# Performance work log

Hardware: AMD Instinct MI355X
Metric: run time of the kernel (lower is better)

Reference implementation:

```python
import jax, jax.numpy as jnp
import numpy as np

B, S, H, E, V, T = 64, 256, 1024, 512, 10000, 64
D = H // 2  # per-direction LSTM hidden


def setup_inputs() -> dict:
    key = jax.random.key(0)
    ks = jax.random.split(key, 16)
    s = jnp.float32(0.02)
    emb = jax.random.normal(ks[4], (V, E), jnp.float32) * s
    emb = emb.at[0].set(0.0)  # padding_idx=0
    return {
        "encoder_outputs": jax.random.normal(ks[0], (B, S, H), jnp.float32),
        "enc_h0": jax.random.normal(ks[1], (2, B, D), jnp.float32),
        "enc_c0": jax.random.normal(ks[2], (2, B, D), jnp.float32),
        "target": jax.random.randint(ks[3], (B, T), 1, V),
        "mask": jnp.zeros((B, S), jnp.bool_),
        "sos_idx": 1,
        "emb": emb,
        "Wa": jax.random.normal(ks[5], (H, H), jnp.float32) * s,
        "Ua": jax.random.normal(ks[6], (H, H), jnp.float32) * s,
        "Va": jax.random.normal(ks[7], (H,), jnp.float32) * s,
        "out_W": jax.random.normal(ks[8], (V, H), jnp.float32) * s,
        "out_b": jnp.zeros((V,), jnp.float32),
        "Wih_f": jax.random.normal(ks[9], (4 * D, E + H), jnp.float32) * s,
        "Whh_f": jax.random.normal(ks[10], (4 * D, D), jnp.float32) * s,
        "bih_f": jnp.zeros((4 * D,), jnp.float32),
        "bhh_f": jnp.zeros((4 * D,), jnp.float32),
        "Wih_b": jax.random.normal(ks[11], (4 * D, E + H), jnp.float32) * s,
        "Whh_b": jax.random.normal(ks[12], (4 * D, D), jnp.float32) * s,
        "bih_b": jnp.zeros((4 * D,), jnp.float32),
        "bhh_b": jnp.zeros((4 * D,), jnp.float32),
    }


def _lstm_cell(x, h, c, Wih, Whh, bih, bhh):
    g = x @ Wih.T + h @ Whh.T + bih + bhh
    i, f, gg, o = jnp.split(g, 4, axis=-1)  # torch gate order i,f,g,o
    c2 = jax.nn.sigmoid(f) * c + jax.nn.sigmoid(i) * jnp.tanh(gg)
    h2 = jax.nn.sigmoid(o) * jnp.tanh(c2)
    return h2, c2


def reference(encoder_outputs, enc_h0, enc_c0, target, mask, sos_idx, emb, Wa, Ua, Va,
              out_W, out_b, Wih_f, Whh_f, bih_f, bhh_f, Wih_b, Whh_b, bih_b, bhh_b):
    # Cache Ua(keys) once (original recomputes it each step; math identical).
    Uk = jnp.einsum('bsh,kh->bsk', encoder_outputs, Ua)  # [B,S,H]
    b = encoder_outputs.shape[0]
    tokens = jnp.concatenate(
        [jnp.full((b, 1), sos_idx, target.dtype), target[:, :-1]], axis=1)  # [B,T]
    xs = tokens.T  # [T,B]

    def step(carry, tok):
        h, c = carry  # each [2,B,D]
        query = jnp.swapaxes(h, 0, 1).reshape(b, -1)  # [B,H] (fwd||bwd)
        sc = jnp.einsum('bsh,h->bs', jnp.tanh((query @ Wa.T)[:, None, :] + Uk), Va)
        sc = jnp.where(mask, -jnp.inf, sc)
        w = jax.nn.softmax(sc, axis=-1)  # [B,S]
        ctx = jnp.einsum('bs,bsh->bh', w, encoder_outputs)  # [B,H]
        x = jnp.concatenate([emb[tok], ctx], axis=-1)  # [B,E+H]
        hf, cf = _lstm_cell(x, h[0], c[0], Wih_f, Whh_f, bih_f, bhh_f)
        hb, cb = _lstm_cell(x, h[1], c[1], Wih_b, Whh_b, bih_b, bhh_b)
        out = jnp.concatenate([hf, hb], axis=-1)  # [B,H]
        logits = out @ out_W.T + out_b  # [B,V]
        return (jnp.stack([hf, hb]), jnp.stack([cf, cb])), (logits, w)

    (h, c), (logits, attns) = jax.lax.scan(step, (enc_h0, enc_c0), xs)
    decoder_outputs = jnp.swapaxes(logits, 0, 1)  # [B,T,V]
    attentions = jnp.swapaxes(attns, 0, 1)        # [B,T,S]
    return decoder_outputs, h, c, attentions
```

## Files before the change

kernel.cpp:

```cpp
#include <hip/hip_runtime.h>

#define NB 64
#define NS 256
#define NH 1024
#define NE 512
#define NV 10000
#define NT 64
#define ND 512
#define NEH 1536
#define HST (65 * NH)

typedef __attribute__((ext_vector_type(8))) short bf16x8;
typedef __attribute__((ext_vector_type(4))) float f32x4;

__device__ __forceinline__ short F2B(float f) {
  unsigned u = __float_as_uint(f);
  return (short)((u + 0x7fffu + ((u >> 16) & 1u)) >> 16);
}
__device__ __forceinline__ float B2F(short s) {
  return __uint_as_float(((unsigned)(unsigned short)s) << 16);
}
__device__ __forceinline__ float ftanh(float x) {
  float e = __expf(2.f * x);
  return 1.f - 2.f * __builtin_amdgcn_rcpf(e + 1.f);
}

#define GLD16(src, dst)                                                        \
  __builtin_amdgcn_global_load_lds(                                            \
      (const __attribute__((address_space(1))) void*)(src),                    \
      (__attribute__((address_space(3))) void*)(dst), 16, 0, 0)

__device__ __forceinline__ void mm64_f32a(
    const float* __restrict__ Af, int lda, const short* __restrict__ Wg,
    int ldw, int K, short* Ch, size_t ldc, char* smem)
{
  const int tid = threadIdx.x;
  const int lane = tid & 63, w = tid >> 6;
  const int qm = (w >> 1) << 5, qn = (w & 1) << 5;
  const int kg = lane >> 4, rl = lane & 15;
  f32x4 acc[2][2] = {};
  const int nIt = K >> 6;

  auto stage = [&](int k0, int buf) {
    char* As = smem + (buf << 14);
    char* Bs = As + 8192;
#pragma unroll
    for (int p = 0; p < 2; ++p) {
      int j = tid + (p << 8);
      int row = j >> 3;
      int c = (j & 7) ^ (row & 7);
      const float* src = Af + (size_t)row * lda + k0 + (c << 3);
      float4 v0 = ((const float4*)src)[0];
      float4 v1 = ((const float4*)src)[1];
      bf16x8 pk;
      pk[0] = F2B(v0.x); pk[1] = F2B(v0.y); pk[2] = F2B(v0.z); pk[3] = F2B(v0.w);
      pk[4] = F2B(v1.x); pk[5] = F2B(v1.y); pk[6] = F2B(v1.z); pk[7] = F2B(v1.w);
      *((bf16x8*)As + j) = pk;
    }
#pragma unroll
    for (int p = 0; p < 2; ++p) {
      int j = (w << 7) + (p << 6) + lane;
      int row = j >> 3;
      int c = (j & 7) ^ (row & 7);
      GLD16(Wg + (size_t)row * ldw + k0 + (c << 3), Bs + (w << 11) + (p << 10));
    }
  };

  stage(0, 0);
  for (int it = 0; it < nIt; ++it) {
    __syncthreads();
    if (it + 1 < nIt) stage((it + 1) << 6, (it + 1) & 1);
    const short* As = (const short*)(smem + ((it & 1) << 14));
    const short* Bs = As + 4096;
#pragma unroll
    for (int kk = 0; kk < 2; ++kk) {
      bf16x8 af[2], bfr[2];
#pragma unroll
      for (int mt = 0; mt < 2; ++mt) {
        int r2 = qm + (mt << 4) + rl;
        int c = (kk << 2) + kg;
        af[mt] = *((const bf16x8*)As + ((r2 << 3) | (c ^ (r2 & 7))));
      }
#pragma unroll
      for (int nt = 0; nt < 2; ++nt) {
        int r2 = qn + (nt << 4) + rl;
        int c = (kk << 2) + kg;
        bfr[nt] = *((const bf16x8*)Bs + ((r2 << 3) | (c ^ (r2 & 7))));
      }
#pragma unroll
      for (int mt = 0; mt < 2; ++mt)
#pragma unroll
        for (int nt = 0; nt < 2; ++nt)
          acc[mt][nt] = __builtin_amdgcn_mfma_f32_16x16x32_bf16(
              af[mt], bfr[nt], acc[mt][nt], 0, 0, 0);
    }
  }
#pragma unroll
  for (int mt = 0; mt < 2; ++mt)
#pragma unroll
    for (int nt = 0; nt < 2; ++nt) {
      int cn = qn + (nt << 4) + rl;
#pragma unroll
      for (int r = 0; r < 4; ++r) {
        int rowm = qm + (mt << 4) + (kg << 2) + r;
        Ch[(size_t)rowm * ldc + cn] = F2B(acc[mt][nt][r]);
      }
    }
}

__global__ __launch_bounds__(256) void uk_mm_f32(const float* __restrict__ enc,
                                                 const short* __restrict__ Ua_h,
                                                 short* __restrict__ Uk_h) {
  __shared__ char smem[32768];
  mm64_f32a(enc + (size_t)blockIdx.y * 64 * NH, NH,
            Ua_h + (size_t)blockIdx.x * 64 * NH, NH, NH,
            Uk_h + (size_t)blockIdx.y * 64 * NH + blockIdx.x * 64, NH, smem);
}

template <int MODE>
__global__ __launch_bounds__(256) void mm128p(
    const short* __restrict__ A, const short* __restrict__ Bw, int nvmax,
    const float* __restrict__ bias, float* __restrict__ Cf,
    short* __restrict__ Ch)
{
  __shared__ char smem[65536];
  const int tid = threadIdx.x, lane = tid & 63, w = tid >> 6;
  const int m0 = blockIdx.y << 7;
  const int n0 = blockIdx.x << 7;
  const int qm = (w >> 1) << 6, qn = (w & 1) << 6;
  const int kg = lane >> 4, rl = lane & 15;
  f32x4 acc[4][4] = {};

  auto stage = [&](int it, int buf) {
    char* dst = smem + (buf << 15);
    const int k0 = it << 6;
#pragma unroll
    for (int p = 0; p < 4; ++p) {
      int j = (((w << 2) + p) << 6) + lane;
      int row = j >> 3;
      int c = (j & 7) ^ (row & 7);
      int m = m0 + row;
      size_t arow = (MODE == 0) ? ((size_t)(m >> 6) * 65 + (m & 63) + 1)
                                : (size_t)m;
      GLD16(A + arow * NH + k0 + (c << 3), dst + (((w << 2) + p) << 10));
      int vr = n0 + row; if (vr > nvmax - 1) vr = nvmax - 1;
      GLD16(Bw + (size_t)vr * NH + k0 + (c << 3),
            dst + 16384 + (((w << 2) + p) << 10));
    }
  };

  stage(0, 0); stage(1, 1);
  for (int it = 0; it < 16; ++it) {
    if (it < 15) asm volatile("s_waitcnt vmcnt(8)" ::: "memory");
    else         asm volatile("s_waitcnt vmcnt(0)" ::: "memory");
    __builtin_amdgcn_s_barrier();
    __builtin_amdgcn_sched_barrier(0);
    const short* As = (const short*)(smem + ((it & 1) << 15));
    const short* Bs = As + 8192;
#pragma unroll
    for (int kk = 0; kk < 2; ++kk) {
      bf16x8 af[4], bfr[4];
#pragma unroll
      for (int mt = 0; mt < 4; ++mt) {
        int r2 = qm + (mt << 4) + rl;
        int c = (kk << 2) + kg;
        af[mt] = *((const bf16x8*)As + ((r2 << 3) | (c ^ (r2 & 7))));
      }
#pragma unroll
      for (int nt = 0; nt < 4; ++nt) {
        int r2 = qn + (nt << 4) + rl;
        int c = (kk << 2) + kg;
        bfr[nt] = *((const bf16x8*)Bs + ((r2 << 3) | (c ^ (r2 & 7))));
      }
#pragma unroll
      for (int mt = 0; mt < 4; ++mt)
#pragma unroll
        for (int nt = 0; nt < 4; ++nt)
          acc[mt][nt] = __builtin_amdgcn_mfma_f32_16x16x32_bf16(
              af[mt], bfr[nt], acc[mt][nt], 0, 0, 0);
    }
    __builtin_amdgcn_sched_barrier(0);
    __builtin_amdgcn_s_barrier();
    if (it + 2 < 16) stage(it + 2, it & 1);
  }
#pragma unroll
  for (int nt = 0; nt < 4; ++nt) {
    int colv = n0 + qn + (nt << 4) + rl;
    if (colv < nvmax) {
#pragma unroll
      for (int mt = 0; mt < 4; ++mt)
#pragma unroll
        for (int r = 0; r < 4; ++r) {
          int m = m0 + qm + (mt << 4) + (kg << 2) + r;
          if (MODE == 0) {
            Cf[(size_t)m * NV + colv] = acc[mt][nt][r] + bias[colv];
          } else {
            Ch[(size_t)m * NH + colv] = F2B(acc[mt][nt][r]);
          }
        }
    }
  }
}

__global__ __launch_bounds__(256) void gates_v2(
    const short* __restrict__ Xt, const short* __restrict__ hcur,
    const short* __restrict__ Wcomb, const float* __restrict__ bperm,
    const float* __restrict__ cq_old, float* __restrict__ hq_f,
    float* __restrict__ cq_new, short* __restrict__ hnext)
{
  __shared__ char smem[61440];
  const int tid = threadIdx.x, lane = tid & 63, w = tid >> 6;
  const int kg = lane >> 4, rl = lane & 15;
  const int dir = blockIdx.x >> 7, gi = blockIdx.x & 127;
  const int hoff = dir << 9;
  const short* Wbase = Wcomb + (((size_t)(dir << 11) + (gi << 4)) << 11);

  auto stage = [&](int it, int buf) {
    char* dst = smem + buf * 20480;
#pragma unroll
    for (int g = 0; g < 4; ++g) {
      int row = (g << 4) + (w << 2) + kg;
      int c = rl ^ (row & 15);
      int k = (it << 7) + (c << 3);
      const short* src = (k < NEH)
          ? (Xt + (size_t)row * NEH + k)
          : (hcur + (size_t)row * HST + hoff + (k - NEH));
      GLD16(src, dst + (g << 12) + (w << 10));
    }
    {
      int rowB = (w << 2) + kg;
      int cB = rl ^ rowB;
      int kB = (it << 7) + (cB << 3);
      GLD16(Wbase + (size_t)rowB * 2048 + kB, dst + 16384 + (w << 10));
    }
  };

  stage(0, 0); stage(1, 1); stage(2, 2);
  f32x4 acc = {};
  int buf = 0;
  for (int it = 0; it < 16; ++it) {
    if (it < 14)      asm volatile("s_waitcnt vmcnt(10)" ::: "memory");
    else if (it == 14) asm volatile("s_waitcnt vmcnt(5)" ::: "memory");
    else               asm volatile("s_waitcnt vmcnt(0)" ::: "memory");
    __builtin_amdgcn_s_barrier();
    __builtin_amdgcn_sched_barrier(0);
    const short* As = (const short*)(smem + buf * 20480);
    const short* Bs = (const short*)(smem + buf * 20480 + 16384);
    const int rowA = (w << 4) + rl;
#pragma unroll
    for (int kk = 0; kk < 4; ++kk) {
      int chunk = (kk << 2) | kg;
      bf16x8 af = *((const bf16x8*)As + ((rowA << 4) | (chunk ^ (rowA & 15))));
      bf16x8 bf = *((const bf16x8*)Bs + ((rl << 4) | (chunk ^ rl)));
      acc = __builtin_amdgcn_mfma_f32_16x16x32_bf16(af, bf, acc, 0, 0, 0);
    }
    __builtin_amdgcn_sched_barrier(0);
    __builtin_amdgcn_s_barrier();
    if (it + 3 < 16) stage(it + 3, buf);
    buf = (buf == 2) ? 0 : buf + 1;
  }
  float* gacc = (float*)smem;
#pragma unroll
  for (int r = 0; r < 4; ++r)
    gacc[((w << 4) + (kg << 2) + r) * 17 + rl] = acc[r];
  __syncthreads();
  {
    const int b = tid >> 2, j2 = tid & 3;
    const float* bp = bperm + (dir << 11) + (gi << 4) + (j2 << 2);
    const float* gr = gacc + b * 17 + (j2 << 2);
    float gi_ = gr[0] + bp[0];
    float gf_ = gr[1] + bp[1];
    float gg_ = gr[2] + bp[2];
    float go_ = gr[3] + bp[3];
    const int d = ((gi >> 2) << 4) + (((gi << 2) + j2) & 15);
    const int idx = (b << 10) + hoff + d;
    float c0v = cq_old[idx];
    float si = 1.f / (1.f + __expf(-gi_));
    float sf = 1.f / (1.f + __expf(-gf_));
    float so = 1.f / (1.f + __expf(-go_));
    float tg = ftanh(gg_);
    float c2 = sf * c0v + si * tg;
    float h2 = so * ftanh(c2);
    hq_f[idx] = h2;
    cq_new[idx] = c2;
    hnext[(size_t)b * HST + hoff + d] = F2B(h2);
  }
}

__global__ __launch_bounds__(256) void q_mm2(const short* __restrict__ hcur,
                                             const short* __restrict__ Wa_h,
                                             float* __restrict__ q)
{
  __shared__ char smem[61440];
  const int tid = threadIdx.x, lane = tid & 63, w = tid >> 6;
  const int kg = lane >> 4, rl = lane & 15;
  const int n0 = blockIdx.x << 4;
  const short* Wbase = Wa_h + (size_t)n0 * NH;

  auto stage = [&](int it, int buf) {
    char* dst = smem + buf * 20480;
#pragma unroll
    for (int g = 0; g < 4; ++g) {
      int row = (g << 4) + (w << 2) + kg;
      int c = rl ^ (row & 15);
      int k = (it << 7) + (c << 3);
      GLD16(hcur + (size_t)row * HST + k, dst + (g << 12) + (w << 10));
    }
    {
      int rowB = (w << 2) + kg;
      int cB = rl ^ rowB;
      int kB = (it << 7) + (cB << 3);
      GLD16(Wbase + (size_t)rowB * NH + kB, dst + 16384 + (w << 10));
    }
  };

  stage(0, 0); stage(1, 1); stage(2, 2);
  f32x4 acc = {};
  int buf = 0;
  for (int it = 0; it < 8; ++it) {
    if (it < 6)       asm volatile("s_waitcnt vmcnt(10)" ::: "memory");
    else if (it == 6) asm volatile("s_waitcnt vmcnt(5)" ::: "memory");
    else              asm volatile("s_waitcnt vmcnt(0)" ::: "memory");
    __builtin_amdgcn_s_barrier();
    __builtin_amdgcn_sched_barrier(0);
    const short* As = (const short*)(smem + buf * 20480);
    const short* Bs = (const short*)(smem + buf * 20480 + 16384);
    const int rowA = (w << 4) + rl;
#pragma unroll
    for (int kk = 0; kk < 4; ++kk) {
      int chunk = (kk << 2) | kg;
      bf16x8 af = *((const bf16x8*)As + ((rowA << 4) | (chunk ^ (rowA & 15))));
      bf16x8 bf = *((const bf16x8*)Bs + ((rl << 4) | (chunk ^ rl)));
      acc = __builtin_amdgcn_mfma_f32_16x16x32_bf16(af, bf, acc, 0, 0, 0);
    }
    __builtin_amdgcn_sched_barrier(0);
    __builtin_amdgcn_s_barrier();
    if (it + 3 < 8) stage(it + 3, buf);
    buf = (buf == 2) ? 0 : buf + 1;
  }
#pragma unroll
  for (int r = 0; r < 4; ++r)
    q[(size_t)((w << 4) + (kg << 2) + r) * NH + n0 + rl] = acc[r];
}

__global__ __launch_bounds__(256) void f2b_k(const float* __restrict__ in,
                                             short* __restrict__ out, int n4) {
  int i = blockIdx.x * 256 + threadIdx.x;
  const int stride = gridDim.x * 256;
  for (; i < n4; i += stride) {
    float4 v = ((const float4*)in)[i];
    short4 o;
    o.x = F2B(v.x); o.y = F2B(v.y); o.z = F2B(v.z); o.w = F2B(v.w);
    ((short4*)out)[i] = o;
  }
}

__global__ __launch_bounds__(256) void f2b2_k(
    const float* __restrict__ in0, short* __restrict__ out0,
    const float* __restrict__ in1, short* __restrict__ out1, int n4each) {
  int i = blockIdx.x * 256 + threadIdx.x;
  const int stride = gridDim.x * 256;
  for (; i < 2 * n4each; i += stride) {
    const float* in = (i < n4each) ? in0 : in1;
    short* out = (i < n4each) ? out0 : out1;
    int j = (i < n4each) ? i : i - n4each;
    float4 v = ((const float4*)in)[j];
    short4 o;
    o.x = F2B(v.x); o.y = F2B(v.y); o.z = F2B(v.z); o.w = F2B(v.w);
    ((short4*)out)[j] = o;
  }
}

__global__ __launch_bounds__(256) void perm_w(
    const float* __restrict__ Wih_f, const float* __restrict__ Whh_f,
    const float* __restrict__ Wih_b, const float* __restrict__ Whh_b,
    const float* __restrict__ bih_f, const float* __restrict__ bhh_f,
    const float* __restrict__ bih_b, const float* __restrict__ bhh_b,
    short* __restrict__ Wcomb, float* __restrict__ bias_perm)
{
  int i = blockIdx.x * 256 + threadIdx.x;
  int k4 = i & 511;
  int np = (i >> 9) & 2047;
  int dir = i >> 20;
  int gate = np & 3, dlo = (np >> 2) & 15, dblk = np >> 6;
  int d = (dblk << 4) + dlo;
  int r = (gate << 9) + d;
  int k = k4 << 2;
  const float* Wih = dir ? Wih_b : Wih_f;
  const float* Whh = dir ? Whh_b : Whh_f;
  float4 v = (k < NEH) ? *(const float4*)(Wih + (size_t)r * NEH + k)
                       : *(const float4*)(Whh + (size_t)r * ND + (k - NEH));
  short4 o;
  o.x = F2B(v.x); o.y = F2B(v.y); o.z = F2B(v.z); o.w = F2B(v.w);
  *(short4*)(Wcomb + ((size_t)((dir << 11) + np) << 11) + k) = o;
  if (k4 == 0) {
    const float* bi = dir ? bih_b : bih_f;
    const float* bh = dir ? bhh_b : bhh_f;
    bias_perm[(dir << 11) + np] = bi[r] + bh[r];
  }
}

__global__ __launch_bounds__(256) void emb_fill(
    const float* __restrict__ emb, const int* __restrict__ target,
    const int* __restrict__ sos, short* __restrict__ Xbuf)
{
  int idx = blockIdx.x * 256 + threadIdx.x;
  int t = idx >> 13;
  int r = idx & 8191;
  int b = r >> 7, e4 = r & 127;
  int tok = (t == 0) ? sos[0] : target[b * NT + t - 1];
  float4 v = *(const float4*)(emb + (size_t)tok * NE + (e4 << 2));
  short4 o;
  o.x = F2B(v.x); o.y = F2B(v.y); o.z = F2B(v.z); o.w = F2B(v.w);
  *(short4*)(Xbuf + (size_t)(t * NB + b) * NEH + (e4 << 2)) = o;
}

__global__ __launch_bounds__(256) void init_state(
    const float* __restrict__ h0, const float* __restrict__ c0,
    float* __restrict__ hq, float* __restrict__ cq, short* __restrict__ H0) {
  int idx = blockIdx.x * 256 + threadIdx.x;
  int b = idx >> 10, dir = (idx >> 9) & 1, d = idx & 511;
  int src = dir * NB * ND + (b << 9) + d;
  float h = h0[src];
  hq[idx] = h;
  cq[idx] = c0[src];
  H0[(size_t)b * HST + (dir << 9) + d] = F2B(h);
}

__global__ __launch_bounds__(256) void final_state(
    const float* __restrict__ hq, const float* __restrict__ cq,
    float* __restrict__ out_h, float* __restrict__ out_c) {
  int idx = blockIdx.x * 256 + threadIdx.x;
  int dir = idx >> 15, r = idx & 32767, b = r >> 9, d = r & 511;
  int src = b * NH + dir * ND + d;
  out_h[idx] = hq[src];
  out_c[idx] = cq[src];
}

__global__ __launch_bounds__(256) void attn_score(
    const float* __restrict__ q, const short* __restrict__ Uk,
    const float* __restrict__ Va, const unsigned char* __restrict__ mask,
    float* __restrict__ sc) {
  __shared__ float qs[NH];
  const int b = blockIdx.x >> 6;
  {
    int t4 = threadIdx.x << 2;
    *(float4*)(qs + t4) = *(const float4*)(q + (size_t)b * NH + t4);
  }
  __syncthreads();
  const int lane = threadIdx.x & 63, wid = threadIdx.x >> 6;
  const int bs = (blockIdx.x << 2) + wid;
  const short* ukp = Uk + (size_t)bs * NH;
  float acc = 0.f;
#pragma unroll
  for (int i = 0; i < 2; ++i) {
    int h = (i << 9) + (lane << 3);
    bf16x8 uv = *(const bf16x8*)(ukp + h);
    float4 q0 = *(const float4*)(qs + h);
    float4 q1 = *(const float4*)(qs + h + 4);
    float4 v0 = *(const float4*)(Va + h);
    float4 v1 = *(const float4*)(Va + h + 4);
    acc += v0.x * ftanh(q0.x + B2F(uv[0]));
    acc += v0.y * ftanh(q0.y + B2F(uv[1]));
    acc += v0.z * ftanh(q0.z + B2F(uv[2]));
    acc += v0.w * ftanh(q0.w + B2F(uv[3]));
    acc += v1.x * ftanh(q1.x + B2F(uv[4]));
    acc += v1.y * ftanh(q1.y + B2F(uv[5]));
    acc += v1.z * ftanh(q1.z + B2F(uv[6]));
    acc += v1.w * ftanh(q1.w + B2F(uv[7]));
  }
#pragma unroll
  for (int o = 32; o; o >>= 1) acc += __shfl_down(acc, o);
  if (lane == 0) sc[bs] = mask[bs] ? -__builtin_inff() : acc;
}

__global__ __launch_bounds__(512) void ctx_soft(
    const float* __restrict__ sc, const short* __restrict__ enc_h,
    const float* __restrict__ enc_f, int use_h,
    short* __restrict__ Xt, float* __restrict__ attn_out, int t) {
  const int tid = threadIdx.x;
  const int b = blockIdx.x >> 2, qh = blockIdx.x & 3;
  __shared__ float red[8];
  __shared__ float ws[NS];
  __shared__ float4 red4[512];
  const int s8 = tid & 255;
  float v = sc[b * NS + s8];
  float m = v;
#pragma unroll
  for (int o = 32; o; o >>= 1) m = fmaxf(m, __shfl_down(m, o));
  if ((tid & 63) == 0) red[tid >> 6] = m;
  __syncthreads();
  m = fmaxf(fmaxf(fmaxf(red[0], red[1]), fmaxf(red[2], red[3])),
            fmaxf(fmaxf(red[4], red[5]), fmaxf(red[6], red[7])));
  float e = __expf(v - m);
  float su = e;
#pragma unroll
  for (int o = 32; o; o >>= 1) su += __shfl_down(su, o);
  __syncthreads();
  if ((tid & 63) == 0) red[tid >> 6] = su;
  __syncthreads();
  su = red[0] + red[1] + red[2] + red[3];
  float wgt = e / su;
  ws[s8] = wgt;
  if (qh == 0 && tid < 256) attn_out[((size_t)b * NT + t) * NS + tid] = wgt;
  __syncthreads();
  const int w8 = tid >> 6, l = tid & 63;
  const int h = (qh << 8) + (l << 2);
  const int s0 = w8 << 5;
  float4 a = make_float4(0.f, 0.f, 0.f, 0.f);
  if (use_h) {
    const short* ep = enc_h + ((size_t)b * NS + s0) * NH + h;
    for (int s = 0; s < 32; ++s) {
      short4 vv = *(const short4*)(ep + (size_t)s * NH);
      float wv = ws[s0 + s];
      a.x += wv * B2F(vv.x); a.y += wv * B2F(vv.y);
      a.z += wv * B2F(vv.z); a.w += wv * B2F(vv.w);
    }
  } else {
    const float* ep = enc_f + ((size_t)b * NS + s0) * NH + h;
    for (int s = 0; s < 32; ++s) {
      float4 vv = *(const float4*)(ep + (size_t)s * NH);
      float wv = ws[s0 + s];
      a.x += wv * vv.x; a.y += wv * vv.y; a.z += wv * vv.z; a.w += wv * vv.w;
    }
  }
  red4[(w8 << 6) + l] = a;
  __syncthreads();
  if (tid < 64) {
    float sx = 0.f, sy = 0.f, sz = 0.f, sw = 0.f;
#pragma unroll
    for (int k = 0; k < 8; ++k) {
      float4 r = red4[(k << 6) + tid];
      sx += r.x; sy += r.y; sz += r.z; sw += r.w;
    }
    short4 o;
    o.x = F2B(sx); o.y = F2B(sy); o.z = F2B(sz); o.w = F2B(sw);
    *(short4*)(Xt + (size_t)b * NEH + NE + (qh << 8) + (tid << 2)) = o;
  }
}

extern "C" void kernel_launch(void* const* d_in, const int* in_sizes, int n_in,
                              void* d_out, int out_size, void* d_ws, size_t ws_size,
                              hipStream_t stream)
{
  const float* enc    = (const float*)d_in[0];
  const float* h0     = (const float*)d_in[1];
  const float* c0     = (const float*)d_in[2];
  const int*   target = (const int*)d_in[3];
  const unsigned char* mask = (const unsigned char*)d_in[4];
  const int*   sos    = (const int*)d_in[5];
  const float* emb    = (const float*)d_in[6];
  const float* Wa     = (const float*)d_in[7];
  const float* Ua     = (const float*)d_in[8];
  const float* Va     = (const float*)d_in[9];
  const float* out_W  = (const float*)d_in[10];
  const float* out_b  = (const float*)d_in[11];
  const float* Wih_f  = (const float*)d_in[12];
  const float* Whh_f  = (const float*)d_in[13];
  const float* bih_f  = (const float*)d_in[14];
  const float* bhh_f  = (const float*)d_in[15];
  const float* Wih_b  = (const float*)d_in[16];
  const float* Whh_b  = (const float*)d_in[17];
  const float* bih_b  = (const float*)d_in[18];
  const float* bhh_b  = (const float*)d_in[19];

  float* out_dec  = (float*)d_out;
  float* out_h    = out_dec + (size_t)NB * NT * NV;
  float* out_c    = out_h + 2 * NB * ND;
  float* out_attn = out_c + 2 * NB * ND;

  char* base = (char*)d_ws;
  size_t off = 0;
  auto alloc = [&](size_t bytes) -> char* {
    char* p = base + off;
    off += (bytes + 255) & ~(size_t)255;
    return p;
  };
  short* Uk_h  = (short*)alloc((size_t)NB * NS * NH * 2);
  short* ow_h  = (short*)alloc((size_t)NV * NH * 2);
  short* Ua_h  = (short*)alloc((size_t)NH * NH * 2);
  short* Wa_h  = (short*)alloc((size_t)NH * NH * 2);
  short* Wcomb = (short*)alloc((size_t)2 * 2048 * 2048 * 2);
  float* bperm = (float*)alloc((size_t)2 * 2048 * 4);
  float* q     = (float*)alloc((size_t)NB * NH * 4);
  float* sc    = (float*)alloc((size_t)NB * NS * 4);
  short* Xbuf  = (short*)alloc((size_t)NT * NB * NEH * 2);
  float* hq    = (float*)alloc((size_t)NB * NH * 4);
  float* cq    = (float*)alloc((size_t)2 * NB * NH * 4);
  short* Hbuf  = (short*)alloc((size_t)NB * HST * 2);
  short* enc_h = nullptr;
  int use_h = 0;
  if (off + (size_t)NB * NS * NH * 2 <= ws_size) {
    enc_h = (short*)alloc((size_t)NB * NS * NH * 2);
    use_h = 1;
  }
  if (off > ws_size) return;

  f2b_k<<<dim3(2048), dim3(256), 0, stream>>>(out_W, ow_h, NV * NH / 4);
  f2b2_k<<<dim3(2048), dim3(256), 0, stream>>>(Ua, Ua_h, Wa, Wa_h, NH * NH / 4);
  perm_w<<<dim3(8192), dim3(256), 0, stream>>>(Wih_f, Whh_f, Wih_b, Whh_b,
                                               bih_f, bhh_f, bih_b, bhh_b,
                                               Wcomb, bperm);
  emb_fill<<<dim3(2048), dim3(256), 0, stream>>>(emb, target, sos, Xbuf);
  init_state<<<dim3(256), dim3(256), 0, stream>>>(h0, c0, hq, cq, Hbuf);
  if (use_h) {
    f2b_k<<<dim3(2048), dim3(256), 0, stream>>>(enc, enc_h, NB * NS * NH / 4);
    mm128p<1><<<dim3(8, 128), dim3(256), 0, stream>>>(enc_h, Ua_h, NH, nullptr,
                                                      nullptr, Uk_h);
  } else {
    uk_mm_f32<<<dim3(16, 256), dim3(256), 0, stream>>>(enc, Ua_h, Uk_h);
  }

  for (int t = 0; t < NT; ++t) {
    const short* hcur = Hbuf + (size_t)t * NH;
    short* hnext = Hbuf + (size_t)(t + 1) * NH;
    float* cq_cur = cq + (t & 1) * (NB * NH);
    float* cq_nxt = cq + ((t & 1) ^ 1) * (NB * NH);
    short* Xt = Xbuf + (size_t)t * NB * NEH;

    q_mm2<<<dim3(64), dim3(256), 0, stream>>>(hcur, Wa_h, q);
    attn_score<<<dim3(4096), dim3(256), 0, stream>>>(q, Uk_h, Va, mask, sc);
    ctx_soft<<<dim3(256), dim3(512), 0, stream>>>(sc, enc_h, enc, use_h,
                                                  Xt, out_attn, t);
    gates_v2<<<dim3(256), dim3(256), 0, stream>>>(Xt, hcur, Wcomb, bperm,
                                                  cq_cur, hq, cq_nxt, hnext);
  }

  mm128p<0><<<dim3(79, 32), dim3(256), 0, stream>>>(Hbuf, ow_h, NV,
                                                    out_b, out_dec, nullptr);
  final_state<<<dim3(256), dim3(256), 0, stream>>>(hq, cq, out_h, out_c);
}
```

Before: 2.127 ms.

## Fuse attention score, softmax and context into one kernel with inter-block barrier

```diff
diff --git a/kernel.cpp b/kernel.cpp
--- a/kernel.cpp
+++ b/kernel.cpp
@@ -125,8 +125,8 @@
 {
   __shared__ char smem[65536];
   const int tid = threadIdx.x, lane = tid & 63, w = tid >> 6;
-  const int m0 = blockIdx.y << 7;
-  const int n0 = blockIdx.x << 7;
+  const int m0 = blockIdx.x << 7;
+  const int n0 = blockIdx.y << 7;
   const int qm = (w >> 1) << 6, qn = (w & 1) << 6;
   const int kg = lane >> 4, rl = lane & 15;
   f32x4 acc[4][4] = {};
@@ -199,6 +199,122 @@
           }
         }
     }
+  }
+}
+
+__global__ __launch_bounds__(512) void attn_one(
+    const float* __restrict__ q, const short* __restrict__ Uk,
+    const float* __restrict__ Va, const unsigned char* __restrict__ mask,
+    const short* __restrict__ enc_h, const float* __restrict__ enc_f,
+    int use_h, short* __restrict__ Xt, float* __restrict__ attn_out,
+    unsigned* __restrict__ ebuf, unsigned* __restrict__ cnt, int t)
+{
+  __shared__ float qs[NH];
+  __shared__ float vas[NH];
+  __shared__ float eall[NS];
+  __shared__ float wsm[NS];
+  __shared__ float4 red4[512];
+  __shared__ float redsum;
+  const int tid = threadIdx.x;
+  const int b = blockIdx.x >> 2, part = blockIdx.x & 3;
+  const int lane = tid & 63, w = tid >> 6;
+
+  {
+    int i2 = tid << 1;
+    *(float2*)(qs + i2) = *(const float2*)(q + (size_t)b * NH + i2);
+    *(float2*)(vas + i2) = *(const float2*)(Va + i2);
+  }
+  __syncthreads();
+
+#pragma unroll 1
+  for (int i = 0; i < 8; ++i) {
+    const int s = (part << 6) + (w << 3) + i;
+    const short* up = Uk + ((size_t)b * NS + s) * NH + (lane << 4);
+    bf16x8 u0 = ((const bf16x8*)up)[0];
+    bf16x8 u1 = ((const bf16x8*)up)[1];
+    const float* qp = qs + (lane << 4);
+    const float* vp = vas + (lane << 4);
+    float a = 0.f;
+#pragma unroll
+    for (int j = 0; j < 8; ++j) a += vp[j] * ftanh(qp[j] + B2F(u0[j]));
+#pragma unroll
+    for (int j = 0; j < 8; ++j) a += vp[8 + j] * ftanh(qp[8 + j] + B2F(u1[j]));
+#pragma unroll
+    for (int o = 32; o; o >>= 1) a += __shfl_down(a, o);
+    if (lane == 0) {
+      float e = mask[b * NS + s] ? 0.f : __expf(a);
+      __hip_atomic_store(&ebuf[b * NS + s], __float_as_uint(e),
+                         __ATOMIC_RELAXED, __HIP_MEMORY_SCOPE_AGENT);
+    }
+  }
+  asm volatile("s_waitcnt vmcnt(0)" ::: "memory");
+  __syncthreads();
+  if (tid == 0) {
+    __hip_atomic_fetch_add(&cnt[b << 4], 1u, __ATOMIC_RELAXED,
+                           __HIP_MEMORY_SCOPE_AGENT);
+    const unsigned tgt = 4u * (unsigned)(t + 1);
+    while (__hip_atomic_load(&cnt[b << 4], __ATOMIC_RELAXED,
+                             __HIP_MEMORY_SCOPE_AGENT) < tgt)
+      __builtin_amdgcn_s_sleep(8);
+  }
+  __syncthreads();
+  if (tid < NS)
+    eall[tid] = __uint_as_float(__hip_atomic_load(
+        &ebuf[b * NS + tid], __ATOMIC_RELAXED, __HIP_MEMORY_SCOPE_AGENT));
+  __syncthreads();
+  if (w == 0) {
+    float su = eall[lane] + eall[lane + 64] + eall[lane + 128] +
+               eall[lane + 192];
+#pragma unroll
+    for (int o = 32; o; o >>= 1) su += __shfl_down(su, o);
+    if (lane == 0) redsum = su;
+  }
+  __syncthreads();
+  {
+    float inv = 1.f / redsum;
+    if (tid < NS) {
+      float ww = eall[tid] * inv;
+      wsm[tid] = ww;
+      if (part == 0) attn_out[((size_t)b * NT + t) * NS + tid] = ww;
+    }
+  }
+  __syncthreads();
+
+  const int w8 = tid >> 6, l = tid & 63;
+  const int h = (part << 8) + (l << 2);
+  const int s0 = w8 << 5;
+  float4 a4 = make_float4(0.f, 0.f, 0.f, 0.f);
+  if (use_h) {
+    const short* ep = enc_h + ((size_t)b * NS + s0) * NH + h;
+#pragma unroll 8
+    for (int s = 0; s < 32; ++s) {
+      short4 vv = *(const short4*)(ep + (size_t)s * NH);
+      float wv = wsm[s0 + s];
+      a4.x += wv * B2F(vv.x); a4.y += wv * B2F(vv.y);
+      a4.z += wv * B2F(vv.z); a4.w += wv * B2F(vv.w);
+    }
+  } else {
+    const float* ep = enc_f + ((size_t)b * NS + s0) * NH + h;
+#pragma unroll 8
+    for (int s = 0; s < 32; ++s) {
+      float4 vv = *(const float4*)(ep + (size_t)s * NH);
+      float wv = wsm[s0 + s];
+      a4.x += wv * vv.x; a4.y += wv * vv.y;
+      a4.z += wv * vv.z; a4.w += wv * vv.w;
+    }
+  }
+  red4[(w8 << 6) + l] = a4;
+  __syncthreads();
+  if (tid < 64) {
+    float sx = 0.f, sy = 0.f, sz = 0.f, sw = 0.f;
+#pragma unroll
+    for (int k = 0; k < 8; ++k) {
+      float4 r = red4[(k << 6) + tid];
+      sx += r.x; sy += r.y; sz += r.z; sw += r.w;
+    }
+    short4 o;
+    o.x = F2B(sx); o.y = F2B(sy); o.z = F2B(sz); o.w = F2B(sw);
+    *(short4*)(Xt + (size_t)b * NEH + NE + (part << 8) + (tid << 2)) = o;
   }
 }
 
@@ -437,108 +553,6 @@
   out_c[idx] = cq[src];
 }
 
-__global__ __launch_bounds__(256) void attn_score(
-    const float* __restrict__ q, const short* __restrict__ Uk,
-    const float* __restrict__ Va, const unsigned char* __restrict__ mask,
-    float* __restrict__ sc) {
-  __shared__ float qs[NH];
-  const int b = blockIdx.x >> 6;
-  {
-    int t4 = threadIdx.x << 2;
-    *(float4*)(qs + t4) = *(const float4*)(q + (size_t)b * NH + t4);
-  }
-  __syncthreads();
-  const int lane = threadIdx.x & 63, wid = threadIdx.x >> 6;
-  const int bs = (blockIdx.x << 2) + wid;
-  const short* ukp = Uk + (size_t)bs * NH;
-  float acc = 0.f;
-#pragma unroll
-  for (int i = 0; i < 2; ++i) {
-    int h = (i << 9) + (lane << 3);
-    bf16x8 uv = *(const bf16x8*)(ukp + h);
-    float4 q0 = *(const float4*)(qs + h);
-    float4 q1 = *(const float4*)(qs + h + 4);
-    float4 v0 = *(const float4*)(Va + h);
-    float4 v1 = *(const float4*)(Va + h + 4);
-    acc += v0.x * ftanh(q0.x + B2F(uv[0]));
-    acc += v0.y * ftanh(q0.y + B2F(uv[1]));
-    acc += v0.z * ftanh(q0.z + B2F(uv[2]));
-    acc += v0.w * ftanh(q0.w + B2F(uv[3]));
-    acc += v1.x * ftanh(q1.x + B2F(uv[4]));
-    acc += v1.y * ftanh(q1.y + B2F(uv[5]));
-    acc += v1.z * ftanh(q1.z + B2F(uv[6]));
-    acc += v1.w * ftanh(q1.w + B2F(uv[7]));
-  }
-#pragma unroll
-  for (int o = 32; o; o >>= 1) acc += __shfl_down(acc, o);
-  if (lane == 0) sc[bs] = mask[bs] ? -__builtin_inff() : acc;
-}
-
-__global__ __launch_bounds__(512) void ctx_soft(
-    const float* __restrict__ sc, const short* __restrict__ enc_h,
-    const float* __restrict__ enc_f, int use_h,
-    short* __restrict__ Xt, float* __restrict__ attn_out, int t) {
-  const int tid = threadIdx.x;
-  const int b = blockIdx.x >> 2, qh = blockIdx.x & 3;
-  __shared__ float red[8];
-  __shared__ float ws[NS];
-  __shared__ float4 red4[512];
-  const int s8 = tid & 255;
-  float v = sc[b * NS + s8];
-  float m = v;
-#pragma unroll
-  for (int o = 32; o; o >>= 1) m = fmaxf(m, __shfl_down(m, o));
-  if ((tid & 63) == 0) red[tid >> 6] = m;
-  __syncthreads();
-  m = fmaxf(fmaxf(fmaxf(red[0], red[1]), fmaxf(red[2], red[3])),
-            fmaxf(fmaxf(red[4], red[5]), fmaxf(red[6], red[7])));
-  float e = __expf(v - m);
-  float su = e;
-#pragma unroll
-  for (int o = 32; o; o >>= 1) su += __shfl_down(su, o);
-  __syncthreads();
-  if ((tid & 63) == 0) red[tid >> 6] = su;
-  __syncthreads();
-  su = red[0] + red[1] + red[2] + red[3];
-  float wgt = e / su;
-  ws[s8] = wgt;
-  if (qh == 0 && tid < 256) attn_out[((size_t)b * NT + t) * NS + tid] = wgt;
-  __syncthreads();
-  const int w8 = tid >> 6, l = tid & 63;
-  const int h = (qh << 8) + (l << 2);
-  const int s0 = w8 << 5;
-  float4 a = make_float4(0.f, 0.f, 0.f, 0.f);
-  if (use_h) {
-    const short* ep = enc_h + ((size_t)b * NS + s0) * NH + h;
-    for (int s = 0; s < 32; ++s) {
-      short4 vv = *(const short4*)(ep + (size_t)s * NH);
-      float wv = ws[s0 + s];
-      a.x += wv * B2F(vv.x); a.y += wv * B2F(vv.y);
-      a.z += wv * B2F(vv.z); a.w += wv * B2F(vv.w);
-    }
-  } else {
-    const float* ep = enc_f + ((size_t)b * NS + s0) * NH + h;
-    for (int s = 0; s < 32; ++s) {
-      float4 vv = *(const float4*)(ep + (size_t)s * NH);
-      float wv = ws[s0 + s];
-      a.x += wv * vv.x; a.y += wv * vv.y; a.z += wv * vv.z; a.w += wv * vv.w;
-    }
-  }
-  red4[(w8 << 6) + l] = a;
-  __syncthreads();
-  if (tid < 64) {
-    float sx = 0.f, sy = 0.f, sz = 0.f, sw = 0.f;
-#pragma unroll
-    for (int k = 0; k < 8; ++k) {
-      float4 r = red4[(k << 6) + tid];
-      sx += r.x; sy += r.y; sz += r.z; sw += r.w;
-    }
-    short4 o;
-    o.x = F2B(sx); o.y = F2B(sy); o.z = F2B(sz); o.w = F2B(sw);
-    *(short4*)(Xt + (size_t)b * NEH + NE + (qh << 8) + (tid << 2)) = o;
-  }
-}
-
 extern "C" void kernel_launch(void* const* d_in, const int* in_sizes, int n_in,
                               void* d_out, int out_size, void* d_ws, size_t ws_size,
                               hipStream_t stream)
@@ -583,7 +597,8 @@
   short* Wcomb = (short*)alloc((size_t)2 * 2048 * 2048 * 2);
   float* bperm = (float*)alloc((size_t)2 * 2048 * 4);
   float* q     = (float*)alloc((size_t)NB * NH * 4);
-  float* sc    = (float*)alloc((size_t)NB * NS * 4);
+  unsigned* ebuf = (unsigned*)alloc((size_t)NB * NS * 4);
+  unsigned* cnt  = (unsigned*)alloc((size_t)NB * 16 * 4);
   short* Xbuf  = (short*)alloc((size_t)NT * NB * NEH * 2);
   float* hq    = (float*)alloc((size_t)NB * NH * 4);
   float* cq    = (float*)alloc((size_t)2 * NB * NH * 4);
@@ -596,6 +611,7 @@
   }
   if (off > ws_size) return;
 
+  hipMemsetAsync(cnt, 0, (size_t)NB * 16 * 4, stream);
   f2b_k<<<dim3(2048), dim3(256), 0, stream>>>(out_W, ow_h, NV * NH / 4);
   f2b2_k<<<dim3(2048), dim3(256), 0, stream>>>(Ua, Ua_h, Wa, Wa_h, NH * NH / 4);
   perm_w<<<dim3(8192), dim3(256), 0, stream>>>(Wih_f, Whh_f, Wih_b, Whh_b,
@@ -605,7 +621,7 @@
   init_state<<<dim3(256), dim3(256), 0, stream>>>(h0, c0, hq, cq, Hbuf);
   if (use_h) {
     f2b_k<<<dim3(2048), dim3(256), 0, stream>>>(enc, enc_h, NB * NS * NH / 4);
-    mm128p<1><<<dim3(8, 128), dim3(256), 0, stream>>>(enc_h, Ua_h, NH, nullptr,
+    mm128p<1><<<dim3(128, 8), dim3(256), 0, stream>>>(enc_h, Ua_h, NH, nullptr,
                                                       nullptr, Uk_h);
   } else {
     uk_mm_f32<<<dim3(16, 256), dim3(256), 0, stream>>>(enc, Ua_h, Uk_h);
@@ -619,14 +635,14 @@
     short* Xt = Xbuf + (size_t)t * NB * NEH;
 
     q_mm2<<<dim3(64), dim3(256), 0, stream>>>(hcur, Wa_h, q);
-    attn_score<<<dim3(4096), dim3(256), 0, stream>>>(q, Uk_h, Va, mask, sc);
-    ctx_soft<<<dim3(256), dim3(512), 0, stream>>>(sc, enc_h, enc, use_h,
-                                                  Xt, out_attn, t);
+    attn_one<<<dim3(256), dim3(512), 0, stream>>>(q, Uk_h, Va, mask,
+                                                  enc_h, enc, use_h, Xt,
+                                                  out_attn, ebuf, cnt, t);
     gates_v2<<<dim3(256), dim3(256), 0, stream>>>(Xt, hcur, Wcomb, bperm,
                                                   cq_cur, hq, cq_nxt, hnext);
   }
 
-  mm128p<0><<<dim3(79, 32), dim3(256), 0, stream>>>(Hbuf, ow_h, NV,
+  mm128p<0><<<dim3(32, 79), dim3(256), 0, stream>>>(Hbuf, ow_h, NV,
                                                     out_b, out_dec, nullptr);
   final_state<<<dim3(256), dim3(256), 0, stream>>>(hq, cq, out_h, out_c);
 }
```

New measurement: 2.223 ms. +4.5%, slower.
